# Performance work log

Hardware: AMD Instinct MI355X
Metric: run time of the kernel (lower is better)

The kernel has to match this reference:

```python
import jax, jax.numpy as jnp
import numpy as np

B, T, D, H = 4, 2048, 1024, 16
HD = D // H          # head_size = 64
FF = 16 * D          # FeedForward hidden = 16*n_embd per source
EPS = 1e-5


def layer_norm(x, g, b):
    mu = jnp.mean(x, axis=-1, keepdims=True)
    var = jnp.mean(jnp.square(x - mu), axis=-1, keepdims=True)
    return (x - mu) * jax.lax.rsqrt(var + EPS) * g + b


def setup_inputs() -> dict:
    key = jax.random.key(0)
    ks = jax.random.split(key, 17)
    s_d = 1.0 / np.sqrt(D)
    s_ff = 1.0 / np.sqrt(FF)
    return {
        "x": jax.random.normal(ks[0], (B, T, D), jnp.float32),
        # per-head Q/K/V linears, batched over heads: [H, D, HD]
        "Wq": jax.random.normal(ks[1], (H, D, HD), jnp.float32) * s_d,
        "bq": jax.random.normal(ks[2], (H, HD), jnp.float32) * s_d,
        "Wk": jax.random.normal(ks[3], (H, D, HD), jnp.float32) * s_d,
        "bk": jax.random.normal(ks[4], (H, HD), jnp.float32) * s_d,
        "Wv": jax.random.normal(ks[5], (H, D, HD), jnp.float32) * s_d,
        "bv": jax.random.normal(ks[6], (H, HD), jnp.float32) * s_d,
        "Wo": jax.random.normal(ks[7], (D, D), jnp.float32) * s_d,
        "bo": jax.random.normal(ks[8], (D,), jnp.float32) * s_d,
        "ln1_g": jnp.ones((D,), jnp.float32),
        "ln1_b": jnp.zeros((D,), jnp.float32),
        "W1": jax.random.normal(ks[9], (D, FF), jnp.float32) * s_d,
        "b1": jax.random.normal(ks[10], (FF,), jnp.float32) * s_d,
        "W2": jax.random.normal(ks[11], (FF, D), jnp.float32) * s_ff,
        "b2": jax.random.normal(ks[12], (D,), jnp.float32) * s_ff,
        "ln2_g": jnp.ones((D,), jnp.float32),
        "ln2_b": jnp.zeros((D,), jnp.float32),
    }


def reference(x, Wq, bq, Wk, bk, Wv, bv, Wo, bo, ln1_g, ln1_b,
              W1, b1, W2, b2, ln2_g, ln2_b):
    # --- multi-head causal self-attention (all heads batched) ---
    q = jnp.einsum('btd,hdk->bhtk', x, Wq) + bq[None, :, None, :]
    k = jnp.einsum('btd,hdk->bhtk', x, Wk) + bk[None, :, None, :]
    v = jnp.einsum('btd,hdk->bhtk', x, Wv) + bv[None, :, None, :]
    scores = jnp.einsum('bhtk,bhsk->bhts', q, k) / np.sqrt(HD)
    causal = jnp.tril(jnp.ones((T, T), bool))
    scores = jnp.where(causal, scores, -jnp.inf)
    attn = jax.nn.softmax(scores, axis=-1)
    out = jnp.einsum('bhts,bhsk->bhtk', attn, v)
    out = out.transpose(0, 2, 1, 3).reshape(x.shape[0], x.shape[1], H * HD)
    attn_out = out @ Wo + bo
    # --- post-LN residual structure, as in the source ---
    out1 = layer_norm(x + attn_out, ln1_g, ln1_b)
    ff = jax.nn.relu(out1 @ W1 + b1) @ W2 + b2
    out2 = layer_norm(out1 + ff, ln2_g, ln2_b)
    return out2
```

## Files before the change

### kernel.cpp

```cpp
#include <hip/hip_runtime.h>

typedef unsigned short u16;
typedef unsigned int   u32;
typedef __attribute__((ext_vector_type(8))) short short8;
typedef __attribute__((ext_vector_type(4))) float f32x4;

#define DEV static __device__ __forceinline__

DEV u16 f2bf(float x) {
  union { float f; u32 u; } c; c.f = x;
  u32 r = c.u + 0x7fffu + ((c.u >> 16) & 1u);
  return (u16)(r >> 16);
}

struct __align__(8) us4 { u16 a, b, c, d; };

DEV void gload16(const void* g, void* l) {
  __builtin_amdgcn_global_load_lds(
      (const __attribute__((address_space(1))) void*)g,
      (__attribute__((address_space(3))) void*)l, 16, 0, 0);
}

template<int EPI>
__global__ __launch_bounds__(256)
void gemm_bt(const u16* __restrict__ A, const u16* __restrict__ Bt,
             const float* __restrict__ bias, const float* __restrict__ resid,
             float* __restrict__ outf, u16* __restrict__ outb,
             u16* __restrict__ q_out, u16* __restrict__ k_out, u16* __restrict__ vt_out,
             int M, int N, int K)
{
  __shared__ __align__(16) u16 As[128 * 64];
  __shared__ __align__(16) u16 Bs[128 * 64];
  const int tid = threadIdx.x;
  const int lane = tid & 63;
  const int wave = tid >> 6;
  const int wm = wave >> 1, wn = wave & 1;
  const int lo = lane & 15, hi = lane >> 4;

  const int nwg = gridDim.x * gridDim.y;
  int bid = blockIdx.y * gridDim.x + blockIdx.x;
  bid = (bid & 7) * (nwg >> 3) + (bid >> 3);
  const int bm = (bid / gridDim.x) * 128;
  const int bn = (bid % gridDim.x) * 128;

  const int kchunk = K / gridDim.z;
  const int kbeg = blockIdx.z * kchunk;
  const int kend = kbeg + kchunk;

  f32x4 zero = {0.f, 0.f, 0.f, 0.f};
  f32x4 acc[4][4];
#pragma unroll
  for (int i = 0; i < 4; ++i)
#pragma unroll
    for (int j = 0; j < 4; ++j) acc[i][j] = zero;

  for (int k0 = kbeg; k0 < kend; k0 += 64) {
#pragma unroll
    for (int i = 0; i < 4; ++i) {
      int slot = i * 4096 + tid * 16;
      int row  = slot >> 7;
      int c16  = (slot >> 4) & 7;
      int gc   = (c16 ^ (row & 7)) * 8;
      gload16(A  + (size_t)(bm + row) * K + k0 + gc,
              (char*)As + i * 4096 + wave * 1024);
      gload16(Bt + (size_t)(bn + row) * K + k0 + gc,
              (char*)Bs + i * 4096 + wave * 1024);
    }
    __syncthreads();
#pragma unroll
    for (int kk = 0; kk < 2; ++kk) {
      short8 a[4], b[4];
      int ks = kk * 4 + hi;
#pragma unroll
      for (int mi = 0; mi < 4; ++mi) {
        int row = wm * 64 + mi * 16 + lo;
        a[mi] = *(const short8*)&As[row * 64 + ((ks ^ (row & 7)) * 8)];
      }
#pragma unroll
      for (int ni = 0; ni < 4; ++ni) {
        int row = wn * 64 + ni * 16 + lo;
        b[ni] = *(const short8*)&Bs[row * 64 + ((ks ^ (row & 7)) * 8)];
      }
#pragma unroll
      for (int mi = 0; mi < 4; ++mi)
#pragma unroll
        for (int ni = 0; ni < 4; ++ni)
          acc[mi][ni] = __builtin_amdgcn_mfma_f32_16x16x32_bf16(
              a[mi], b[ni], acc[mi][ni], 0, 0, 0);
    }
    __syncthreads();
  }

#pragma unroll
  for (int mi = 0; mi < 4; ++mi) {
#pragma unroll
    for (int ni = 0; ni < 4; ++ni) {
      int col = bn + wn * 64 + ni * 16 + lo;
#pragma unroll
      for (int r = 0; r < 4; ++r) {
        int row = bm + wm * 64 + mi * 16 + hi * 4 + r;
        float v = acc[mi][ni][r];
        if (EPI == 0) {
          v += bias[col];
          int qkv = col >> 10, wc = col & 1023, h = wc >> 6, hd = wc & 63;
          int b_ = row >> 11, t = row & 2047;
          u16 bv = f2bf(v);
          if (qkv == 0)
            q_out[((size_t)((b_ * 16 + h) * 2048 + t)) * 64 + hd] = bv;
          else if (qkv == 1)
            k_out[((size_t)((b_ * 16 + h) * 2048 + t)) * 64 + hd] = bv;
          else
            vt_out[((size_t)((b_ * 16 + h) * 64 + hd)) * 2048 + t] = bv;
        } else if (EPI == 1) {
          v += bias[col] + resid[(size_t)row * N + col];
          outf[(size_t)row * N + col] = v;
        } else if (EPI == 2) {
          v += bias[col];
          v = v > 0.f ? v : 0.f;
          outb[(size_t)row * N + col] = f2bf(v);
        } else {
          atomicAdd(&outf[(size_t)row * N + col], v);
        }
      }
    }
  }
}

__global__ __launch_bounds__(256)
void attn_kernel(const u16* __restrict__ Q, const u16* __restrict__ Kb,
                 const u16* __restrict__ Vt, u16* __restrict__ O)
{
  __shared__ __align__(16) u16 Pl[4][16 * 80];
  const int tid = threadIdx.x, lane = tid & 63, w = tid >> 6;
  const int lo = lane & 15, hi = lane >> 4;
  const int bh = blockIdx.y;
  const int qt = gridDim.x - 1 - blockIdx.x;
  const int q0 = qt * 64;

  const size_t qbase = ((size_t)bh * 2048 + q0 + w * 16 + lo) * 64;
  short8 qf[2];
  qf[0] = *(const short8*)(Q + qbase + hi * 8);
  qf[1] = *(const short8*)(Q + qbase + 32 + hi * 8);

  const u16* kbase = Kb + ((size_t)bh * 2048 + lo) * 64 + hi * 8;
  const u16* vbase = Vt + ((size_t)bh * 64 + lo) * 2048 + hi * 8;

  float m[4]    = {-1e30f, -1e30f, -1e30f, -1e30f};
  float lsum[4] = {0.f, 0.f, 0.f, 0.f};
  f32x4 zero = {0.f, 0.f, 0.f, 0.f};
  f32x4 oacc[4];
#pragma unroll
  for (int i = 0; i < 4; ++i) oacc[i] = zero;

  const int smax = qt;
  for (int s = 0; s <= smax; ++s) {
    const u16* kp = kbase + (size_t)s * 64 * 64;

    f32x4 sacc[4];
#pragma unroll
    for (int i = 0; i < 4; ++i) sacc[i] = zero;
#pragma unroll
    for (int ni = 0; ni < 4; ++ni) {
      short8 kf0 = *(const short8*)(kp + ni * 1024);
      short8 kf1 = *(const short8*)(kp + ni * 1024 + 32);
      sacc[ni] = __builtin_amdgcn_mfma_f32_16x16x32_bf16(qf[0], kf0, sacc[ni], 0, 0, 0);
      sacc[ni] = __builtin_amdgcn_mfma_f32_16x16x32_bf16(qf[1], kf1, sacc[ni], 0, 0, 0);
    }

    const bool diag = (s == smax);
    float pvv[4][4];
#pragma unroll
    for (int r = 0; r < 4; ++r) {
      int qrow = q0 + w * 16 + hi * 4 + r;
      float mx = -1e30f;
#pragma unroll
      for (int ni = 0; ni < 4; ++ni) {
        float v = sacc[ni][r] * 0.125f;
        int kv = s * 64 + ni * 16 + lo;
        if (diag && kv > qrow) v = -1e30f;
        pvv[ni][r] = v;
        mx = fmaxf(mx, v);
      }
#pragma unroll
      for (int msk = 1; msk < 16; msk <<= 1) mx = fmaxf(mx, __shfl_xor(mx, msk));
      float mnew = fmaxf(m[r], mx);
      float corr = __expf(m[r] - mnew);
      m[r] = mnew;
      float rs = 0.f;
#pragma unroll
      for (int ni = 0; ni < 4; ++ni) {
        float p = __expf(pvv[ni][r] - mnew);
        pvv[ni][r] = p;
        rs += p;
      }
#pragma unroll
      for (int msk = 1; msk < 16; msk <<= 1) rs += __shfl_xor(rs, msk);
      lsum[r] = lsum[r] * corr + rs;
#pragma unroll
      for (int nd = 0; nd < 4; ++nd) oacc[nd][r] *= corr;
    }

#pragma unroll
    for (int ni = 0; ni < 4; ++ni) {
      int chunk = ni * 2 + (lo >> 3);
      int wi    = lo & 7;
#pragma unroll
      for (int r = 0; r < 4; ++r) {
        int rowp = hi * 4 + r;
        Pl[w][rowp * 80 + (((chunk ^ (rowp & 7)) << 3) | wi)] = f2bf(pvv[ni][r]);
      }
    }

#pragma unroll
    for (int kk = 0; kk < 2; ++kk) {
      short8 pa = *(const short8*)&Pl[w][lo * 80 + (((kk * 4 + hi) ^ (lo & 7)) << 3)];
#pragma unroll
      for (int nd = 0; nd < 4; ++nd) {
        short8 vf = *(const short8*)(vbase + (size_t)nd * 16 * 2048 + s * 64 + kk * 32);
        oacc[nd] = __builtin_amdgcn_mfma_f32_16x16x32_bf16(pa, vf, oacc[nd], 0, 0, 0);
      }
    }
  }

  const int b_ = bh >> 4, h_ = bh & 15;
#pragma unroll
  for (int r = 0; r < 4; ++r) {
    int t = q0 + w * 16 + hi * 4 + r;
    float inv = 1.f / lsum[r];
    size_t base = ((size_t)b_ * 2048 + t) * 1024 + h_ * 64;
#pragma unroll
    for (int nd = 0; nd < 4; ++nd)
      O[base + nd * 16 + lo] = f2bf(oacc[nd][r] * inv);
  }
}

__global__ __launch_bounds__(256)
void ln_kernel(const float* __restrict__ in, const float* __restrict__ g,
               const float* __restrict__ bp, float* __restrict__ outf,
               u16* __restrict__ outb,
               float* __restrict__ seed_out, const float* __restrict__ seed_bias)
{
  const int row = blockIdx.x, t = threadIdx.x;
  const f32x4 v = *(const f32x4*)(in + (size_t)row * 1024 + t * 4);
  float s  = v[0] + v[1] + v[2] + v[3];
  float sq = v[0] * v[0] + v[1] * v[1] + v[2] * v[2] + v[3] * v[3];
#pragma unroll
  for (int off = 32; off; off >>= 1) {
    s  += __shfl_down(s, off);
    sq += __shfl_down(sq, off);
  }
  __shared__ float red[8];
  const int lane = t & 63, w = t >> 6;
  if (lane == 0) { red[w] = s; red[4 + w] = sq; }
  __syncthreads();
  s  = red[0] + red[1] + red[2] + red[3];
  sq = red[4] + red[5] + red[6] + red[7];
  float mu  = s * (1.f / 1024.f);
  float var = sq * (1.f / 1024.f) - mu * mu;
  float rstd = rsqrtf(var + 1e-5f);
  const f32x4 gv = *(const f32x4*)(g + t * 4);
  const f32x4 bv = *(const f32x4*)(bp + t * 4);
  f32x4 o;
#pragma unroll
  for (int j = 0; j < 4; ++j) o[j] = (v[j] - mu) * rstd * gv[j] + bv[j];
  *(f32x4*)(outf + (size_t)row * 1024 + t * 4) = o;
  if (outb) {
    us4 ob = {f2bf(o[0]), f2bf(o[1]), f2bf(o[2]), f2bf(o[3])};
    *(us4*)(outb + (size_t)row * 1024 + t * 4) = ob;
  }
  if (seed_out) {
    const f32x4 sb = *(const f32x4*)(seed_bias + t * 4);
    f32x4 so = {o[0] + sb[0], o[1] + sb[1], o[2] + sb[2], o[3] + sb[3]};
    *(f32x4*)(seed_out + (size_t)row * 1024 + t * 4) = so;
  }
}

__global__ __launch_bounds__(256)
void cvt_bf16(const float* __restrict__ src, u16* __restrict__ dst, int n4)
{
  int i = blockIdx.x * 256 + threadIdx.x;
  if (i < n4) {
    f32x4 v = *(const f32x4*)(src + (size_t)i * 4);
    us4 o = {f2bf(v[0]), f2bf(v[1]), f2bf(v[2]), f2bf(v[3])};
    *(us4*)(dst + (size_t)i * 4) = o;
  }
}

__global__ __launch_bounds__(256)
void transpose_cvt(const float* __restrict__ src, u16* __restrict__ dst, int R, int C)
{
  __shared__ float tile[64][65];
  const int c0 = blockIdx.x * 64, r0 = blockIdx.y * 64;
  const int t = threadIdx.x;
  const int rl = t >> 4, c4 = (t & 15) * 4;
#pragma unroll
  for (int i = 0; i < 4; ++i) {
    f32x4 v = *(const f32x4*)(src + (size_t)(r0 + rl + i * 16) * C + c0 + c4);
    tile[rl + i * 16][c4 + 0] = v[0];
    tile[rl + i * 16][c4 + 1] = v[1];
    tile[rl + i * 16][c4 + 2] = v[2];
    tile[rl + i * 16][c4 + 3] = v[3];
  }
  __syncthreads();
#pragma unroll
  for (int j = 0; j < 16; ++j) {
    int o = t + j * 256;
    int c = o >> 6, r = o & 63;
    dst[(size_t)(c0 + c) * R + r0 + r] = f2bf(tile[r][c]);
  }
}

__global__ __launch_bounds__(256)
void qkv_pack(const float* __restrict__ Wq, const float* __restrict__ Wk,
              const float* __restrict__ Wv, u16* __restrict__ Wt)
{
  const float* src = blockIdx.z == 0 ? Wq : (blockIdx.z == 1 ? Wk : Wv);
  src += (size_t)blockIdx.y * 1024 * 64;
  __shared__ float tile[64][65];
  const int k0 = blockIdx.x * 64;
  const int t = threadIdx.x;
  const int rl = t >> 4, c4 = (t & 15) * 4;
#pragma unroll
  for (int i = 0; i < 4; ++i) {
    f32x4 v = *(const f32x4*)(src + (size_t)(k0 + rl + i * 16) * 64 + c4);
    tile[rl + i * 16][c4 + 0] = v[0];
    tile[rl + i * 16][c4 + 1] = v[1];
    tile[rl + i * 16][c4 + 2] = v[2];
    tile[rl + i * 16][c4 + 3] = v[3];
  }
  __syncthreads();
  size_t nbase = (size_t)blockIdx.z * 1024 + blockIdx.y * 64;
#pragma unroll
  for (int j = 0; j < 16; ++j) {
    int o = t + j * 256;
    int hd = o >> 6, r = o & 63;
    Wt[(nbase + hd) * 1024 + k0 + r] = f2bf(tile[r][hd]);
  }
}

__global__ void bias_pack(const float* __restrict__ bq, const float* __restrict__ bk,
                          const float* __restrict__ bv, float* __restrict__ out)
{
  int i = blockIdx.x * 256 + threadIdx.x;
  if (i < 3072) {
    const float* s = (i >> 10) == 0 ? bq : ((i >> 10) == 1 ? bk : bv);
    out[i] = s[i & 1023];
  }
}

extern "C" void kernel_launch(void* const* d_in, const int* in_sizes, int n_in,
                              void* d_out, int out_size, void* d_ws, size_t ws_size,
                              hipStream_t stream)
{
  const float* x    = (const float*)d_in[0];
  const float* Wq   = (const float*)d_in[1];
  const float* bq   = (const float*)d_in[2];
  const float* Wk   = (const float*)d_in[3];
  const float* bk   = (const float*)d_in[4];
  const float* Wv   = (const float*)d_in[5];
  const float* bv   = (const float*)d_in[6];
  const float* Wo   = (const float*)d_in[7];
  const float* bo   = (const float*)d_in[8];
  const float* ln1g = (const float*)d_in[9];
  const float* ln1b = (const float*)d_in[10];
  const float* W1   = (const float*)d_in[11];
  const float* b1   = (const float*)d_in[12];
  const float* W2   = (const float*)d_in[13];
  const float* b2   = (const float*)d_in[14];
  const float* ln2g = (const float*)d_in[15];
  const float* ln2b = (const float*)d_in[16];
  float* out = (float*)d_out;

  char* ws = (char*)d_ws;
  const size_t MB = 1ull << 20;
  u16*   Wqkvt = (u16*)(ws + 0);
  float* bqkv  = (float*)(ws + 6 * MB);
  u16*   Wot   = (u16*)(ws + 7 * MB);
  u16*   W1t   = (u16*)(ws + 9 * MB);
  u16*   W2t   = (u16*)(ws + 41 * MB);
  u16*   out1b = (u16*)(ws + 73 * MB);
  float* y1    = (float*)(ws + 89 * MB);
  u16*   Xb    = (u16*)(ws + 121 * MB);
  u16*   Qb    = (u16*)(ws + 137 * MB);
  u16*   Kb    = (u16*)(ws + 153 * MB);
  u16*   Vt    = (u16*)(ws + 169 * MB);
  u16*   attnb = (u16*)(ws + 185 * MB);
  u16*   h_buf = (u16*)(ws + 121 * MB);
  float* y2    = out;

  const int nchunks = (ws_size >= 377 * MB) ? 1 : 4;
  const int Mc      = 8192 / nchunks;
  const int zsplit  = (nchunks == 1) ? 4 : 8;

  cvt_bf16<<<8192, 256, 0, stream>>>(x, Xb, 8192 * 1024 / 4);
  qkv_pack<<<dim3(16, 16, 3), 256, 0, stream>>>(Wq, Wk, Wv, Wqkvt);
  bias_pack<<<12, 256, 0, stream>>>(bq, bk, bv, bqkv);
  transpose_cvt<<<dim3(16, 16), 256, 0, stream>>>(Wo, Wot, 1024, 1024);
  transpose_cvt<<<dim3(256, 16), 256, 0, stream>>>(W1, W1t, 1024, 16384);
  transpose_cvt<<<dim3(16, 256), 256, 0, stream>>>(W2, W2t, 16384, 1024);

  gemm_bt<0><<<dim3(24, 64), 256, 0, stream>>>(Xb, Wqkvt, bqkv, nullptr,
      nullptr, nullptr, Qb, Kb, Vt, 8192, 3072, 1024);

  attn_kernel<<<dim3(32, 64), 256, 0, stream>>>(Qb, Kb, Vt, attnb);

  gemm_bt<1><<<dim3(8, 64), 256, 0, stream>>>(attnb, Wot, bo, x,
      y1, nullptr, nullptr, nullptr, nullptr, 8192, 1024, 1024);

  ln_kernel<<<8192, 256, 0, stream>>>(y1, ln1g, ln1b, y1, out1b, y2, b2);

  for (int c = 0; c < nchunks; ++c) {
    gemm_bt<2><<<dim3(128, Mc / 128), 256, 0, stream>>>(
        out1b + (size_t)c * Mc * 1024, W1t, b1, nullptr,
        nullptr, h_buf, nullptr, nullptr, nullptr, Mc, 16384, 1024);
    gemm_bt<3><<<dim3(8, Mc / 128, zsplit), 256, 0, stream>>>(
        h_buf, W2t, nullptr, nullptr,
        y2 + (size_t)c * Mc * 1024, nullptr, nullptr, nullptr, nullptr,
        Mc, 1024, 16384);
  }

  ln_kernel<<<8192, 256, 0, stream>>>(y2, ln2g, ln2b, out, nullptr,
                                      nullptr, nullptr);

  (void)in_sizes; (void)n_in; (void)out_size;
}
```

Measured before the change: 1.746 ms.

## Double-buffer K/V tiles in LDS via async global-to-LDS loads in attention

The attention kernel used to have each wave load its K and V fragments straight from global memory in every key block. It now stages each 64x64 K and V^T tile into XOR-swizzled shared memory with global_load_lds, double-buffered so the next tile loads while the current one is computed. The block shares each tile across its four waves instead of every wave fetching it separately. In exchange it adds 32KB of LDS, which may lower occupancy, plus two barriers per iteration and hand-written vmcnt waits whose correctness depends on how the compiler orders memory ops.

```diff
diff --git a/kernel.cpp b/kernel.cpp
--- a/kernel.cpp
+++ b/kernel.cpp
@@ -130,6 +130,8 @@
 void attn_kernel(const u16* __restrict__ Q, const u16* __restrict__ Kb,
                  const u16* __restrict__ Vt, u16* __restrict__ O)
 {
+  __shared__ __align__(16) u16 Ks[2][64 * 64];
+  __shared__ __align__(16) u16 Vs[2][64 * 64];
   __shared__ __align__(16) u16 Pl[4][16 * 80];
   const int tid = threadIdx.x, lane = tid & 63, w = tid >> 6;
   const int lo = lane & 15, hi = lane >> 4;
@@ -142,8 +144,30 @@
   qf[0] = *(const short8*)(Q + qbase + hi * 8);
   qf[1] = *(const short8*)(Q + qbase + 32 + hi * 8);
 
-  const u16* kbase = Kb + ((size_t)bh * 2048 + lo) * 64 + hi * 8;
-  const u16* vbase = Vt + ((size_t)bh * 64 + lo) * 2048 + hi * 8;
+  const int slot0 = tid * 16;
+  const int srow0 = slot0 >> 7;
+  const int sgc0  = (((slot0 >> 4) & 7) ^ (srow0 & 7)) * 8;
+  const int slot1 = 4096 + tid * 16;
+  const int srow1 = slot1 >> 7;
+  const int sgc1  = (((slot1 >> 4) & 7) ^ (srow1 & 7)) * 8;
+  const u16* kRow0 = Kb + ((size_t)bh * 2048 + srow0) * 64 + sgc0;
+  const u16* kRow1 = Kb + ((size_t)bh * 2048 + srow1) * 64 + sgc1;
+  const u16* vRow0 = Vt + ((size_t)bh * 64 + srow0) * 2048 + sgc0;
+  const u16* vRow1 = Vt + ((size_t)bh * 64 + srow1) * 2048 + sgc1;
+  const int ldsOff = tid * 16 - (tid * 16 & 4095) ? 0 : 0;
+
+#define ATTN_STAGE(buf, s)                                                   \
+  do {                                                                       \
+    gload16(kRow0 + (size_t)(s) * 64 * 64,                                   \
+            (char*)Ks + (buf) * 8192 + ((tid * 16) & 4095) +                 \
+            ((tid * 16) >> 12) * 0);                                         \
+    gload16(kRow1 + (size_t)(s) * 64 * 64,                                   \
+            (char*)Ks + (buf) * 8192 + 4096 + ((tid * 16) & 4095));          \
+    gload16(vRow0 + (size_t)(s) * 64,                                        \
+            (char*)Vs + (buf) * 8192 + ((tid * 16) & 4095));                 \
+    gload16(vRow1 + (size_t)(s) * 64,                                        \
+            (char*)Vs + (buf) * 8192 + 4096 + ((tid * 16) & 4095));          \
+  } while (0)
 
   float m[4]    = {-1e30f, -1e30f, -1e30f, -1e30f};
   float lsum[4] = {0.f, 0.f, 0.f, 0.f};
@@ -153,19 +177,32 @@
   for (int i = 0; i < 4; ++i) oacc[i] = zero;
 
   const int smax = qt;
+  ATTN_STAGE(0, 0);
+  int cur = 0;
+
   for (int s = 0; s <= smax; ++s) {
-    const u16* kp = kbase + (size_t)s * 64 * 64;
+    if (s < smax) {
+      ATTN_STAGE(cur ^ 1, s + 1);
+      asm volatile("s_waitcnt vmcnt(4)" ::: "memory");
+    } else {
+      asm volatile("s_waitcnt vmcnt(0)" ::: "memory");
+    }
+    __builtin_amdgcn_s_barrier();
+
+    const u16* ksb = Ks[cur];
+    const u16* vsb = Vs[cur];
 
     f32x4 sacc[4];
 #pragma unroll
     for (int i = 0; i < 4; ++i) sacc[i] = zero;
 #pragma unroll
-    for (int ni = 0; ni < 4; ++ni) {
-      short8 kf0 = *(const short8*)(kp + ni * 1024);
-      short8 kf1 = *(const short8*)(kp + ni * 1024 + 32);
-      sacc[ni] = __builtin_amdgcn_mfma_f32_16x16x32_bf16(qf[0], kf0, sacc[ni], 0, 0, 0);
-      sacc[ni] = __builtin_amdgcn_mfma_f32_16x16x32_bf16(qf[1], kf1, sacc[ni], 0, 0, 0);
-    }
+    for (int ni = 0; ni < 4; ++ni)
+#pragma unroll
+      for (int kk = 0; kk < 2; ++kk) {
+        int row = ni * 16 + lo;
+        short8 kf = *(const short8*)&ksb[row * 64 + (((kk * 4 + hi) ^ (row & 7)) * 8)];
+        sacc[ni] = __builtin_amdgcn_mfma_f32_16x16x32_bf16(qf[kk], kf, sacc[ni], 0, 0, 0);
+      }
 
     const bool diag = (s == smax);
     float pvv[4][4];
@@ -216,11 +253,15 @@
       short8 pa = *(const short8*)&Pl[w][lo * 80 + (((kk * 4 + hi) ^ (lo & 7)) << 3)];
 #pragma unroll
       for (int nd = 0; nd < 4; ++nd) {
-        short8 vf = *(const short8*)(vbase + (size_t)nd * 16 * 2048 + s * 64 + kk * 32);
+        int row = nd * 16 + lo;
+        short8 vf = *(const short8*)&vsb[row * 64 + (((kk * 4 + hi) ^ (row & 7)) * 8)];
         oacc[nd] = __builtin_amdgcn_mfma_f32_16x16x32_bf16(pa, vf, oacc[nd], 0, 0, 0);
       }
     }
-  }
+    __builtin_amdgcn_s_barrier();
+    cur ^= 1;
+  }
+#undef ATTN_STAGE
 
   const int b_ = bh >> 4, h_ = bh & 15;
 #pragma unroll
@@ -232,6 +273,7 @@
     for (int nd = 0; nd < 4; ++nd)
       O[base + nd * 16 + lo] = f2bf(oacc[nd][r] * inv);
   }
+  (void)ldsOff;
 }
 
 __global__ __launch_bounds__(256)
```

After: 1.485 ms. 1.18x faster.
